# Kernel optimization log

Hardware: AMD Instinct MI355X
Metric: run time of the kernel (lower is better)

The kernel has to match this reference:

```python
import jax, jax.numpy as jnp
import numpy as np

N = 100000
E = 3200000
IN_DIM = 256
HID = 128
HID2 = 64
K = 16


def setup_inputs() -> dict:
    key = jax.random.key(0)
    ks = jax.random.split(key, 12)
    x = jax.random.normal(ks[0], (N, IN_DIM), dtype=jnp.float32)
    edge_index = jax.random.randint(ks[1], (2, E), 0, N, dtype=jnp.int64)
    edge_weight = jax.random.uniform(ks[2], (E,), dtype=jnp.float32)
    s = lambda f: 1.0 / np.sqrt(f)
    W0 = jax.random.normal(ks[3], (IN_DIM, HID), dtype=jnp.float32) * s(IN_DIM)
    b0 = jnp.zeros((HID,), jnp.float32)
    P0w = jax.random.normal(ks[4], (IN_DIM, HID), dtype=jnp.float32) * s(IN_DIM)
    P0b = jnp.zeros((HID,), jnp.float32)
    W1 = jax.random.normal(ks[5], (HID, HID2), dtype=jnp.float32) * s(HID)
    b1 = jnp.zeros((HID2,), jnp.float32)
    P1w = jax.random.normal(ks[6], (HID, HID2), dtype=jnp.float32) * s(HID)
    P1b = jnp.zeros((HID2,), jnp.float32)
    W2 = jax.random.normal(ks[7], (HID2, K), dtype=jnp.float32) * s(HID2)
    b2 = jnp.zeros((K,), jnp.float32)
    return {"x": x, "edge_index": edge_index, "edge_weight": edge_weight,
            "W0": W0, "b0": b0, "P0w": P0w, "P0b": P0b,
            "W1": W1, "b1": b1, "P1w": P1w, "P1b": P1b,
            "W2": W2, "b2": b2}


def _gcn_norm(edge_index, edge_weight, n):
    # add self loops (weight 1), symmetric normalization per PyG gcn_norm
    loop = jnp.arange(n, dtype=edge_index.dtype)
    row = jnp.concatenate([edge_index[0], loop])
    col = jnp.concatenate([edge_index[1], loop])
    w = jnp.concatenate([edge_weight, jnp.ones((n,), edge_weight.dtype)])
    deg = jax.ops.segment_sum(w, col, num_segments=n)
    dinv = jnp.where(deg > 0, jax.lax.rsqrt(deg), 0.0)
    return row, col, dinv[row] * w * dinv[col]


def reference(x, edge_index, edge_weight, W0, b0, P0w, P0b, W1, b1, P1w, P1b, W2, b2):
    n = x.shape[0]
    row, col, nw = _gcn_norm(edge_index, edge_weight, n)

    def gcn(h, W, b):
        hW = h @ W  # transform first (PyG GCNConv), then scatter-aggregate
        agg = jax.ops.segment_sum(nw[:, None] * hW[row], col, num_segments=n)
        return agg + b

    # layer 0: skip is Linear(input_dim, hidden); dropout = identity (eval)
    h = jax.nn.selu(gcn(x, W0, b0) + (x @ P0w + P0b))
    # layer 1: skip is Linear(hidden, hidden//2)
    h = jax.nn.selu(gcn(h, W1, b1) + (h @ P1w + P1b))
    # layer 2: no skip, no dropout
    h = jax.nn.selu(gcn(h, W2, b2))
    return jax.nn.softmax(h, axis=-1)
```

## Files before the change

### kernel.cpp

```cpp
#include <hip/hip_runtime.h>
#include <hip/hip_fp16.h>
#include <cmath>

#define IN_DIM 256
#define HID 128
#define HID2 64
#define SB 256
#define NODES_PB 128
#define NB_MAX 1024
#define BCAP 4608

struct __align__(8) EdgeP { int s; float w; };
union H4 { __half h[4]; uint2 u; };
union H2 { __half2 h2; uint u; };

using f16x8 = __attribute__((ext_vector_type(8))) _Float16;
using f32x4 = __attribute__((ext_vector_type(4))) float;

__device__ __forceinline__ float selu_f(float x) {
    const float scale = 1.0507009873554805f;
    const float alpha = 1.6732632423543772f;
    return x > 0.f ? scale * x : scale * alpha * expm1f(x);
}


__global__ void zero_ints(int* p, int n) {
    int i = blockIdx.x * blockDim.x + threadIdx.x;
    if (i < n) p[i] = 0;
}

__global__ void transpose_w(const float* __restrict__ B1, const float* __restrict__ B2,
                            __half* __restrict__ WT, int K, int C1, int C2) {
    int c = blockIdx.x;
    for (int k = threadIdx.x; k < K; k += blockDim.x) {
        float v = (c < C1) ? B1[(size_t)k * C1 + c] : B2[(size_t)k * C2 + (c - C1)];
        WT[(size_t)c * K + k] = __float2half(v);
    }
}

__global__ void deg_dinv(const EdgeP* __restrict__ ell, int* cnt, float* dinv, int n, int cap) {
    int wid = (blockIdx.x * blockDim.x + threadIdx.x) >> 6;
    int lane = threadIdx.x & 63;
    if (wid >= n) return;
    size_t base = (size_t)wid * cap;
    int len = min(cnt[wid], cap);
    float s = 0.f;
    for (int i = lane; i < len; i += 64) s += ell[base + i].w;
#pragma unroll
    for (int o = 32; o; o >>= 1) s += __shfl_xor(s, o);
    if (lane == 0) {
        dinv[wid] = rsqrtf(s + 1.0f);
        cnt[wid] = len;
    }
}

__global__ __launch_bounds__(256) void bin_gemm0(
    const float* __restrict__ A, const __half* __restrict__ WT,
    const float* __restrict__ bias1, const float* __restrict__ bias2,
    __half* __restrict__ outA, float* __restrict__ outB, int M,
    const int* __restrict__ ei, const float* __restrict__ ew,
    int* cnt_or_bcur, EdgeP* __restrict__ dst_buf,
    int E, int cap, int epb, int sblocks, int nb, int mode) {
    const int tid = threadIdx.x;
    __shared__ __align__(16) __half sA16[128 * 40];
    __shared__ __align__(16) __half sB16[128 * 40];

    if ((int)blockIdx.x < sblocks) {
        int lo = blockIdx.x * epb;
        int hi = min(E, lo + epb);
        if (mode == 1) {
            int* hist = (int*)sA16;
            int* gbase = (int*)sB16;
            for (int i = tid; i < nb; i += 256) hist[i] = 0;
            __syncthreads();
            for (int e = lo + tid; e < hi; e += 256)
                atomicAdd(&hist[ei[E + e] >> 7], 1);
            __syncthreads();
            for (int b = tid; b < nb; b += 256) {
                int h = hist[b];
                gbase[b] = h ? atomicAdd(&cnt_or_bcur[b], h) : 0;
                hist[b] = 0;
            }
            __syncthreads();
            for (int e = lo + tid; e < hi; e += 256) {
                int d = ei[E + e];
                int s = ei[e];
                float w = ew[e];
                int b = d >> 7;
                int lp = atomicAdd(&hist[b], 1);
                int off = gbase[b] + lp;
                if (off < BCAP) {
                    EdgeP p; p.s = (s << 7) | (d & 127); p.w = w;
                    dst_buf[(size_t)b * BCAP + off] = p;
                }
            }
        } else {
            for (int base = lo; base < hi; base += 2048) {
                int r[8], c[8], pos[8];
                float wv[8];
#pragma unroll
                for (int j = 0; j < 8; ++j) {
                    int e = base + j * 256 + tid;
                    c[j] = -1;
                    if (e < hi) { r[j] = ei[e]; c[j] = ei[E + e]; wv[j] = ew[e]; }
                }
#pragma unroll
                for (int j = 0; j < 8; ++j)
                    if (c[j] >= 0) pos[j] = atomicAdd(&cnt_or_bcur[c[j]], 1);
#pragma unroll
                for (int j = 0; j < 8; ++j)
                    if (c[j] >= 0 && pos[j] < cap) {
                        EdgeP p; p.s = r[j]; p.w = wv[j];
                        dst_buf[(size_t)c[j] * cap + pos[j]] = p;
                    }
            }
        }
        return;
    }

    const int bid = blockIdx.x - sblocks;
    const int m0 = (bid >> 1) * 128;
    const int n0 = (bid & 1) * 128;
    const int lane = tid & 63;
    const int wv = tid >> 6;
    const int wr = (wv >> 1) * 64;
    const int wc = (wv & 1) * 64;
    const int lr = lane & 15, lk = lane >> 4;

    f32x4 zero = {0.f, 0.f, 0.f, 0.f};
    f32x4 acc[4][4];
#pragma unroll
    for (int i = 0; i < 4; ++i)
#pragma unroll
        for (int j = 0; j < 4; ++j) acc[i][j] = zero;

    for (int k0 = 0; k0 < IN_DIM; k0 += 32) {
#pragma unroll
        for (int p = 0; p < 4; ++p) {
            int f4 = p * 256 + tid;
            int r = f4 >> 3;
            int kk = (f4 & 7) << 2;
            int row = m0 + r;
            float4 v = make_float4(0.f, 0.f, 0.f, 0.f);
            if (row < M) v = *(const float4*)(A + (size_t)row * IN_DIM + k0 + kk);
            H4 h;
            h.h[0] = __float2half(v.x); h.h[1] = __float2half(v.y);
            h.h[2] = __float2half(v.z); h.h[3] = __float2half(v.w);
            *(uint2*)&sA16[r * 40 + kk] = h.u;
        }
#pragma unroll
        for (int p = 0; p < 2; ++p) {
            int f = p * 256 + tid;
            int c = f >> 2;
            int kc = (f & 3) << 3;
            *(uint4*)&sB16[c * 40 + kc] =
                *(const uint4*)(WT + (size_t)(n0 + c) * IN_DIM + k0 + kc);
        }
        __syncthreads();
        f16x8 af[4], bf[4];
#pragma unroll
        for (int i = 0; i < 4; ++i)
            af[i] = *(const f16x8*)&sA16[(wr + i * 16 + lr) * 40 + lk * 8];
#pragma unroll
        for (int j = 0; j < 4; ++j)
            bf[j] = *(const f16x8*)&sB16[(wc + j * 16 + lr) * 40 + lk * 8];
#pragma unroll
        for (int i = 0; i < 4; ++i)
#pragma unroll
            for (int j = 0; j < 4; ++j)
                acc[i][j] = __builtin_amdgcn_mfma_f32_16x16x32_f16(af[i], bf[j], acc[i][j], 0, 0, 0);
        __syncthreads();
    }

    float bs[4];
    if (n0 != 0) {
#pragma unroll
        for (int j = 0; j < 4; ++j) {
            int c = wc + j * 16 + lr;
            bs[j] = bias1[c] + bias2[c];
        }
    }
#pragma unroll
    for (int i = 0; i < 4; ++i) {
        int rowb = m0 + wr + i * 16 + lk * 4;
#pragma unroll
        for (int j = 0; j < 4; ++j) {
            int col = wc + j * 16 + lr;
#pragma unroll
            for (int r = 0; r < 4; ++r) {
                int row = rowb + r;
                if (row < M) {
                    if (n0 == 0)
                        outA[(size_t)row * HID + col] = __float2half(acc[i][j][r]);
                    else
                        outB[(size_t)row * HID + col] = acc[i][j][r] + bs[j];
                }
            }
        }
    }
}

__global__ __launch_bounds__(256) void bucket_build(
    const EdgeP* __restrict__ recs, const int* __restrict__ bcur,
    EdgeP* __restrict__ ell, int* __restrict__ cnt, float* __restrict__ dinv,
    int n, int cap) {
    __shared__ int lcnt[NODES_PB];
    __shared__ float ldeg[NODES_PB];
    int b = blockIdx.x, tid = threadIdx.x;
    if (tid < NODES_PB) { lcnt[tid] = 0; ldeg[tid] = 0.f; }
    __syncthreads();
    int m = min(bcur[b], BCAP);
    const EdgeP* r = recs + (size_t)b * BCAP;
    for (int i = tid; i < m; i += 256) {
        EdgeP p = r[i];
        int dl = p.s & 127;
        int s = p.s >> 7;
        int pos = atomicAdd(&lcnt[dl], 1);
        atomicAdd(&ldeg[dl], p.w);
        if (pos < cap) {
            EdgeP q; q.s = s; q.w = p.w;
            ell[((size_t)(b * NODES_PB + dl)) * cap + pos] = q;
        }
    }
    __syncthreads();
    if (tid < NODES_PB) {
        int v = b * NODES_PB + tid;
        if (v < n) {
            cnt[v] = min(lcnt[tid], cap);
            dinv[v] = rsqrtf(ldeg[tid] + 1.0f);
        }
    }
}

__global__ __launch_bounds__(256) void gemm1_fused(
    const float* __restrict__ A, const __half* __restrict__ WT,
    const float* __restrict__ bias1, const float* __restrict__ bias2,
    __half* __restrict__ outA, float* __restrict__ outB, int M) {
    const int tid = threadIdx.x;
    __shared__ __align__(16) __half sA16[128 * 40];
    __shared__ __align__(16) __half sB16[128 * 40];
    const int m0 = blockIdx.x * 128;
    const int lane = tid & 63;
    const int wv = tid >> 6;
    const int wr = (wv >> 1) * 64;
    const int wc = (wv & 1) * 64;
    const int lr = lane & 15, lk = lane >> 4;

    f32x4 zero = {0.f, 0.f, 0.f, 0.f};
    f32x4 acc[4][4];
#pragma unroll
    for (int i = 0; i < 4; ++i)
#pragma unroll
        for (int j = 0; j < 4; ++j) acc[i][j] = zero;

    for (int k0 = 0; k0 < HID; k0 += 32) {
#pragma unroll
        for (int p = 0; p < 4; ++p) {
            int f4 = p * 256 + tid;
            int r = f4 >> 3;
            int kk = (f4 & 7) << 2;
            int row = m0 + r;
            float4 v = make_float4(0.f, 0.f, 0.f, 0.f);
            if (row < M) v = *(const float4*)(A + (size_t)row * HID + k0 + kk);
            H4 h;
            h.h[0] = __float2half(v.x); h.h[1] = __float2half(v.y);
            h.h[2] = __float2half(v.z); h.h[3] = __float2half(v.w);
            *(uint2*)&sA16[r * 40 + kk] = h.u;
        }
#pragma unroll
        for (int p = 0; p < 2; ++p) {
            int f = p * 256 + tid;
            int c = f >> 2;
            int kc = (f & 3) << 3;
            *(uint4*)&sB16[c * 40 + kc] =
                *(const uint4*)(WT + (size_t)c * HID + k0 + kc);
        }
        __syncthreads();
        f16x8 af[4], bf[4];
#pragma unroll
        for (int i = 0; i < 4; ++i)
            af[i] = *(const f16x8*)&sA16[(wr + i * 16 + lr) * 40 + lk * 8];
#pragma unroll
        for (int j = 0; j < 4; ++j)
            bf[j] = *(const f16x8*)&sB16[(wc + j * 16 + lr) * 40 + lk * 8];
#pragma unroll
        for (int i = 0; i < 4; ++i)
#pragma unroll
            for (int j = 0; j < 4; ++j)
                acc[i][j] = __builtin_amdgcn_mfma_f32_16x16x32_f16(af[i], bf[j], acc[i][j], 0, 0, 0);
        __syncthreads();
    }

    float bs[4];
    if (wc != 0) {
#pragma unroll
        for (int j = 0; j < 4; ++j) {
            int c = wc + j * 16 + lr - HID2;
            bs[j] = bias1[c] + bias2[c];
        }
    }
#pragma unroll
    for (int i = 0; i < 4; ++i) {
        int rowb = m0 + wr + i * 16 + lk * 4;
#pragma unroll
        for (int j = 0; j < 4; ++j) {
            int col = wc + j * 16 + lr;
#pragma unroll
            for (int r = 0; r < 4; ++r) {
                int row = rowb + r;
                if (row < M) {
                    if (wc == 0)
                        outA[(size_t)row * HID2 + col] = __float2half(acc[i][j][r]);
                    else
                        outB[(size_t)row * HID2 + (col - HID2)] = acc[i][j][r] + bs[j];
                }
            }
        }
    }
}

__global__ __launch_bounds__(256) void aggregate128(
    const __half* __restrict__ hW, float* __restrict__ S,
    const float* __restrict__ dinv, const int* __restrict__ cnt,
    const EdgeP* __restrict__ ell, int cap, int n) {
    int v = (blockIdx.x * 256 + threadIdx.x) >> 6;
    int lane = threadIdx.x & 63;
    if (v >= n) return;
    float di = dinv[v];
    float2 sv = *(const float2*)&S[(size_t)v * HID + lane * 2];
    H2 selfh; selfh.u = *(const uint*)&hW[(size_t)v * HID + lane * 2];
    float2 selff = __half22float2(selfh.h2);
    float selfx = sv.x + di * di * selff.x;
    float selfy = sv.y + di * di * selff.y;

    size_t base = (size_t)v * cap;
    int len = cnt[v];
    float ax[4] = {0.f, 0.f, 0.f, 0.f};
    float ay[4] = {0.f, 0.f, 0.f, 0.f};
    int i = 0;
    for (; i + 8 <= len; i += 8) {
        EdgeP p[8];
        float dv[8];
        uint h[8];
#pragma unroll
        for (int j = 0; j < 8; ++j) p[j] = ell[base + i + j];
#pragma unroll
        for (int j = 0; j < 8; ++j) {
            dv[j] = dinv[p[j].s];
            h[j] = *(const uint*)&hW[(size_t)p[j].s * HID + lane * 2];
        }
#pragma unroll
        for (int j = 0; j < 8; ++j) {
            float t = dv[j] * p[j].w;
            H2 hh; hh.u = h[j];
            float2 hf = __half22float2(hh.h2);
            ax[j & 3] = fmaf(t, hf.x, ax[j & 3]);
            ay[j & 3] = fmaf(t, hf.y, ay[j & 3]);
        }
    }
    for (; i < len; ++i) {
        EdgeP p = ell[base + i];
        float t = dinv[p.s] * p.w;
        H2 hh; hh.u = *(const uint*)&hW[(size_t)p.s * HID + lane * 2];
        float2 hf = __half22float2(hh.h2);
        ax[0] = fmaf(t, hf.x, ax[0]);
        ay[0] = fmaf(t, hf.y, ay[0]);
    }
    float sx = selfx + di * ((ax[0] + ax[1]) + (ax[2] + ax[3]));
    float sy = selfy + di * ((ay[0] + ay[1]) + (ay[2] + ay[3]));
    *(float2*)&S[(size_t)v * HID + lane * 2] = make_float2(selu_f(sx), selu_f(sy));
}

__global__ __launch_bounds__(256) void agg64_gemm2(
    const __half* __restrict__ hW, const float* __restrict__ S,
    const float* __restrict__ dinv, const int* __restrict__ cnt,
    const EdgeP* __restrict__ ell, int cap,
    const float* __restrict__ W2, __half* __restrict__ out16, int n) {
    __shared__ float sW[64 * 16];
    __shared__ float sh[4][64];
    int tid = threadIdx.x;
#pragma unroll
    for (int i = 0; i < 4; ++i) sW[i * 256 + tid] = W2[i * 256 + tid];

    int g = tid >> 6, f = tid & 63;
    int v = blockIdx.x * 4 + g;
    if (v < n) {
        float di = dinv[v];
        float self = S[(size_t)v * 64 + f] + di * di * __half2float(hW[(size_t)v * 64 + f]);
        size_t base = (size_t)v * cap;
        int len = cnt[v];
        float a[4] = {0.f, 0.f, 0.f, 0.f};
        int i = 0;
        for (; i + 8 <= len; i += 8) {
            EdgeP p[8];
            float dv[8];
            __half hv[8];
#pragma unroll
            for (int j = 0; j < 8; ++j) p[j] = ell[base + i + j];
#pragma unroll
            for (int j = 0; j < 8; ++j) {
                dv[j] = dinv[p[j].s];
                hv[j] = hW[(size_t)p[j].s * 64 + f];
            }
#pragma unroll
            for (int j = 0; j < 8; ++j)
                a[j & 3] = fmaf(dv[j] * p[j].w, __half2float(hv[j]), a[j & 3]);
        }
        for (; i < len; ++i) {
            EdgeP p = ell[base + i];
            a[0] = fmaf(dinv[p.s] * p.w, __half2float(hW[(size_t)p.s * 64 + f]), a[0]);
        }
        sh[g][f] = selu_f(self + di * ((a[0] + a[1]) + (a[2] + a[3])));
    }
    __syncthreads();
    if (v < n && f < 16) {
        float acc = 0.f;
#pragma unroll
        for (int k = 0; k < 64; ++k) acc = fmaf(sh[g][k], sW[k * 16 + f], acc);
        out16[(size_t)v * 16 + f] = __float2half(acc);
    }
}

__global__ __launch_bounds__(256) void agg_softmax(
    const __half* __restrict__ hW, const float* __restrict__ b2,
    const float* __restrict__ dinv, const int* __restrict__ cnt,
    const EdgeP* __restrict__ ell, int cap,
    float* __restrict__ out, int n) {
    int tid = threadIdx.x;
    int g = tid >> 4, f = tid & 15;
    int v = blockIdx.x * 16 + g;
    if (v >= n) return;
    float di = dinv[v];
    float acc = b2[f] + di * di * __half2float(hW[(size_t)v * 16 + f]);
    size_t base = (size_t)v * cap;
    int len = cnt[v];
    float a[4] = {0.f, 0.f, 0.f, 0.f};
    int i = 0;
    for (; i + 4 <= len; i += 4) {
        EdgeP p[4];
        float dv[4];
        __half hv[4];
#pragma unroll
        for (int j = 0; j < 4; ++j) p[j] = ell[base + i + j];
#pragma unroll
        for (int j = 0; j < 4; ++j) {
            dv[j] = dinv[p[j].s];
            hv[j] = hW[(size_t)p[j].s * 16 + f];
        }
#pragma unroll
        for (int j = 0; j < 4; ++j)
            a[j] = fmaf(dv[j] * p[j].w, __half2float(hv[j]), a[j]);
    }
    for (; i < len; ++i) {
        EdgeP p = ell[base + i];
        a[0] = fmaf(dinv[p.s] * p.w, __half2float(hW[(size_t)p.s * 16 + f]), a[0]);
    }
    acc += di * ((a[0] + a[1]) + (a[2] + a[3]));
    acc = selu_f(acc);
    float m = acc;
    m = fmaxf(m, __shfl_xor(m, 1));
    m = fmaxf(m, __shfl_xor(m, 2));
    m = fmaxf(m, __shfl_xor(m, 4));
    m = fmaxf(m, __shfl_xor(m, 8));
    float ex = expf(acc - m);
    float sm = ex;
    sm += __shfl_xor(sm, 1);
    sm += __shfl_xor(sm, 2);
    sm += __shfl_xor(sm, 4);
    sm += __shfl_xor(sm, 8);
    out[(size_t)v * 16 + f] = ex / sm;
}

extern "C" void kernel_launch(void* const* d_in, const int* in_sizes, int n_in,
                              void* d_out, int out_size, void* d_ws, size_t ws_size,
                              hipStream_t stream) {
    const float* x = (const float*)d_in[0];
    const int* ei = (const int*)d_in[1];
    const float* ew = (const float*)d_in[2];
    const float* W0 = (const float*)d_in[3];
    const float* b0 = (const float*)d_in[4];
    const float* P0w = (const float*)d_in[5];
    const float* P0b = (const float*)d_in[6];
    const float* W1 = (const float*)d_in[7];
    const float* b1 = (const float*)d_in[8];
    const float* P1w = (const float*)d_in[9];
    const float* P1b = (const float*)d_in[10];
    const float* W2 = (const float*)d_in[11];
    const float* b2 = (const float*)d_in[12];
    float* out = (float*)d_out;
    const int n = in_sizes[0] / IN_DIM;
    const int E = in_sizes[2];
    const int NB = (n + NODES_PB - 1) / NODES_PB;

    auto al = [](size_t b) { return (b + 255) & ~(size_t)255; };
    size_t oCnt = 0;
    size_t oDinv = oCnt + al((size_t)n * 4);
    size_t oBcur = oDinv + al((size_t)n * 4);
    size_t oWT0 = oBcur + al((size_t)NB_MAX * 4);
    size_t oWT1 = oWT0 + al((size_t)IN_DIM * (HID * 2) * 2);
    size_t oA = oWT1 + al((size_t)HID * HID * 2);
    size_t oB = oA + al((size_t)n * HID * 2);
    size_t oEll = oB + al((size_t)n * HID * 4);
    size_t szEll96 = al((size_t)n * 96 * 8);
    size_t szEll80 = al((size_t)n * 80 * 8);
    size_t szRec = al((size_t)NB * BCAP * 8);
    size_t szCD = al((size_t)n * HID2 * 4) + al((size_t)n * 16 * 2);
    size_t szR = szRec > szCD ? szRec : szCD;

    int cap;
    int mode;
    if (NB <= NB_MAX && oEll + szEll96 + szR <= ws_size) { cap = 96; mode = 1; }
    else if (oEll + szEll96 + szCD <= ws_size) { cap = 96; mode = 0; }
    else { cap = 80; mode = 0; }

    char* base = (char*)d_ws;
    int* cnt = (int*)(base + oCnt);
    float* dinv = (float*)(base + oDinv);
    int* bcur = (int*)(base + oBcur);
    __half* WT0 = (__half*)(base + oWT0);
    __half* WT1 = (__half*)(base + oWT1);
    __half* bufA = (__half*)(base + oA);
    float* bufB = (float*)(base + oB);
    EdgeP* ell = (EdgeP*)(base + oEll);
    size_t oR = oEll + (cap == 96 ? szEll96 : szEll80);
    EdgeP* recs = (EdgeP*)(base + oR);
    float* bufC = (float*)(base + oR);
    __half* bufD = (__half*)(base + oR + al((size_t)n * HID2 * 4));

    int gx = (n + 127) / 128;
    int gemmBlocks = gx * 2;
    int epb = (E + SB - 1) / SB;

    transpose_w<<<2 * HID, 128, 0, stream>>>(W0, P0w, WT0, IN_DIM, HID, HID);
    transpose_w<<<HID, 128, 0, stream>>>(W1, P1w, WT1, HID, HID2, HID2);

    if (mode == 1) {
        zero_ints<<<(NB_MAX + 255) / 256, 256, 0, stream>>>(bcur, NB_MAX);
        bin_gemm0<<<SB + gemmBlocks, 256, 0, stream>>>(
            x, WT0, b0, P0b, bufA, bufB, n, ei, ew, bcur, recs,
            E, cap, epb, SB, NB, 1);
        bucket_build<<<NB, 256, 0, stream>>>(recs, bcur, ell, cnt, dinv, n, cap);
    } else {
        zero_ints<<<(n + 255) / 256, 256, 0, stream>>>(cnt, n);
        bin_gemm0<<<SB + gemmBlocks, 256, 0, stream>>>(
            x, WT0, b0, P0b, bufA, bufB, n, ei, ew, cnt, ell,
            E, cap, epb, SB, NB, 0);
        int nbW = (n * 64 + 255) / 256;
        deg_dinv<<<nbW, 256, 0, stream>>>(ell, cnt, dinv, n, cap);
    }

    aggregate128<<<(n * 64 + 255) / 256, 256, 0, stream>>>(bufA, bufB, dinv, cnt, ell, cap, n);

    gemm1_fused<<<gx, 256, 0, stream>>>(bufB, WT1, b1, P1b, bufA, bufC, n);

    agg64_gemm2<<<(n + 3) / 4, 256, 0, stream>>>(bufA, bufC, dinv, cnt, ell, cap, W2, bufD, n);
    agg_softmax<<<(n + 15) / 16, 256, 0, stream>>>(bufD, b2, dinv, cnt, ell, cap, out, n);
}
```

Measured before the change: 512.0 us.

## Locally counting-sort edge chunks in LDS before scattering to buckets and ELL

The binning pass now processes edges in chunks of 4096, builds a per-chunk histogram, exclusive-scans it in one wave, and counting-sorts records in LDS so each bucket's records are written contiguously to global memory. Buckets double in size (256 nodes each), and bucket_build applies the same chunked local sort so ELL writes per node are grouped. The aim is to turn random scattered global writes into coalesced runs. The cost is extra LDS traffic, more barriers, and roughly 48KB of shared memory in bin_gemm0, which lowers occupancy for the GEMM blocks in the same kernel.

Result: faster. 495.7 us (-3.2%).

```diff
diff --git a/kernel.cpp b/kernel.cpp
--- a/kernel.cpp
+++ b/kernel.cpp
@@ -6,9 +6,10 @@
 #define HID 128
 #define HID2 64
 #define SB 256
-#define NODES_PB 128
-#define NB_MAX 1024
-#define BCAP 4608
+#define NODES_PB 256
+#define NBKT_MAX 448
+#define BCAP 9216
+#define CH 4096
 
 struct __align__(8) EdgeP { int s; float w; };
 union H4 { __half h[4]; uint2 u; };
@@ -54,6 +55,33 @@
     }
 }
 
+template <int PER>
+__device__ __forceinline__ void wave0_excl_scan(const int* lds_in, int* lds_out, int nb, int tid) {
+    if (tid < 64) {
+        int r[PER];
+        int sum = 0;
+#pragma unroll
+        for (int k = 0; k < PER; ++k) {
+            int idx = tid * PER + k;
+            int v = (idx < nb) ? lds_in[idx] : 0;
+            r[k] = sum;
+            sum += v;
+        }
+        int run = sum;
+#pragma unroll
+        for (int o = 1; o < 64; o <<= 1) {
+            int t = __shfl_up(run, o);
+            if (tid >= o) run += t;
+        }
+        int excl = run - sum;
+#pragma unroll
+        for (int k = 0; k < PER; ++k) {
+            int idx = tid * PER + k;
+            if (idx < nb) lds_out[idx] = excl + r[k];
+        }
+    }
+}
+
 __global__ __launch_bounds__(256) void bin_gemm0(
     const float* __restrict__ A, const __half* __restrict__ WT,
     const float* __restrict__ bias1, const float* __restrict__ bias2,
@@ -62,37 +90,53 @@
     int* cnt_or_bcur, EdgeP* __restrict__ dst_buf,
     int E, int cap, int epb, int sblocks, int nb, int mode) {
     const int tid = threadIdx.x;
-    __shared__ __align__(16) __half sA16[128 * 40];
-    __shared__ __align__(16) __half sB16[128 * 40];
+    __shared__ __align__(16) char smem[48128];
 
     if ((int)blockIdx.x < sblocks) {
         int lo = blockIdx.x * epb;
         int hi = min(E, lo + epb);
         if (mode == 1) {
-            int* hist = (int*)sA16;
-            int* gbase = (int*)sB16;
-            for (int i = tid; i < nb; i += 256) hist[i] = 0;
-            __syncthreads();
-            for (int e = lo + tid; e < hi; e += 256)
-                atomicAdd(&hist[ei[E + e] >> 7], 1);
-            __syncthreads();
-            for (int b = tid; b < nb; b += 256) {
-                int h = hist[b];
-                gbase[b] = h ? atomicAdd(&cnt_or_bcur[b], h) : 0;
-                hist[b] = 0;
-            }
-            __syncthreads();
-            for (int e = lo + tid; e < hi; e += 256) {
-                int d = ei[E + e];
-                int s = ei[e];
-                float w = ew[e];
-                int b = d >> 7;
-                int lp = atomicAdd(&hist[b], 1);
-                int off = gbase[b] + lp;
-                if (off < BCAP) {
-                    EdgeP p; p.s = (s << 7) | (d & 127); p.w = w;
-                    dst_buf[(size_t)b * BCAP + off] = p;
+            int* hist = (int*)smem;
+            int* off = hist + NBKT_MAX;
+            int* cur = off + NBKT_MAX;
+            int* gbase = cur + NBKT_MAX;
+            int* sortedS = gbase + NBKT_MAX;
+            float* sortedW = (float*)(sortedS + CH);
+            short* smap = (short*)(sortedW + CH);
+            for (int c0 = lo; c0 < hi; c0 += CH) {
+                int cn = min(CH, hi - c0);
+                for (int i = tid; i < nb; i += 256) hist[i] = 0;
+                __syncthreads();
+                for (int r = tid; r < cn; r += 256)
+                    atomicAdd(&hist[ei[E + c0 + r] >> 8], 1);
+                __syncthreads();
+                wave0_excl_scan<7>(hist, off, nb, tid);
+                __syncthreads();
+                for (int b = tid; b < nb; b += 256) {
+                    int h = hist[b];
+                    gbase[b] = h ? atomicAdd(&cnt_or_bcur[b], h) : 0;
+                    cur[b] = off[b];
                 }
+                __syncthreads();
+                for (int r = tid; r < cn; r += 256) {
+                    int e = c0 + r;
+                    int d = ei[E + e];
+                    int b = d >> 8;
+                    int slot = atomicAdd(&cur[b], 1);
+                    sortedS[slot] = (ei[e] << 8) | (d & 255);
+                    sortedW[slot] = ew[e];
+                    smap[slot] = (short)b;
+                }
+                __syncthreads();
+                for (int i = tid; i < cn; i += 256) {
+                    int b = smap[i];
+                    int addr = gbase[b] + (i - off[b]);
+                    if (addr < BCAP) {
+                        EdgeP p; p.s = sortedS[i]; p.w = sortedW[i];
+                        dst_buf[(size_t)b * BCAP + addr] = p;
+                    }
+                }
+                __syncthreads();
             }
         } else {
             for (int base = lo; base < hi; base += 2048) {
@@ -118,6 +162,8 @@
         return;
     }
 
+    __half* sA16 = (__half*)smem;
+    __half* sB16 = (__half*)(smem + 10240);
     const int bid = blockIdx.x - sblocks;
     const int m0 = (bid >> 1) * 128;
     const int n0 = (bid & 1) * 128;
@@ -206,29 +252,58 @@
     int n, int cap) {
     __shared__ int lcnt[NODES_PB];
     __shared__ float ldeg[NODES_PB];
+    __shared__ int chist[NODES_PB];
+    __shared__ int coff[NODES_PB];
+    __shared__ int ccur[NODES_PB];
+    __shared__ __align__(8) int sortedS[CH];
+    __shared__ float sortedW[CH];
+    __shared__ unsigned char cmap[CH];
     int b = blockIdx.x, tid = threadIdx.x;
-    if (tid < NODES_PB) { lcnt[tid] = 0; ldeg[tid] = 0.f; }
+    lcnt[tid] = 0;
+    ldeg[tid] = 0.f;
     __syncthreads();
     int m = min(bcur[b], BCAP);
-    const EdgeP* r = recs + (size_t)b * BCAP;
-    for (int i = tid; i < m; i += 256) {
-        EdgeP p = r[i];
-        int dl = p.s & 127;
-        int s = p.s >> 7;
-        int pos = atomicAdd(&lcnt[dl], 1);
-        atomicAdd(&ldeg[dl], p.w);
-        if (pos < cap) {
-            EdgeP q; q.s = s; q.w = p.w;
-            ell[((size_t)(b * NODES_PB + dl)) * cap + pos] = q;
-        }
-    }
-    __syncthreads();
-    if (tid < NODES_PB) {
-        int v = b * NODES_PB + tid;
-        if (v < n) {
-            cnt[v] = min(lcnt[tid], cap);
-            dinv[v] = rsqrtf(ldeg[tid] + 1.0f);
-        }
+    const EdgeP* rbase = recs + (size_t)b * BCAP;
+    for (int c0 = 0; c0 < m; c0 += CH) {
+        int cn = min(CH, m - c0);
+        chist[tid] = 0;
+        __syncthreads();
+        for (int i = tid; i < cn; i += 256) {
+            EdgeP p = rbase[c0 + i];
+            int dl = p.s & 255;
+            atomicAdd(&chist[dl], 1);
+            atomicAdd(&ldeg[dl], p.w);
+        }
+        __syncthreads();
+        wave0_excl_scan<4>(chist, coff, NODES_PB, tid);
+        __syncthreads();
+        ccur[tid] = coff[tid];
+        __syncthreads();
+        for (int i = tid; i < cn; i += 256) {
+            EdgeP p = rbase[c0 + i];
+            int dl = p.s & 255;
+            int slot = atomicAdd(&ccur[dl], 1);
+            sortedS[slot] = p.s >> 8;
+            sortedW[slot] = p.w;
+            cmap[slot] = (unsigned char)dl;
+        }
+        __syncthreads();
+        for (int i = tid; i < cn; i += 256) {
+            int dl = cmap[i];
+            int rank = lcnt[dl] + (i - coff[dl]);
+            if (rank < cap) {
+                EdgeP q; q.s = sortedS[i]; q.w = sortedW[i];
+                ell[((size_t)(b * NODES_PB + dl)) * cap + rank] = q;
+            }
+        }
+        __syncthreads();
+        lcnt[tid] += chist[tid];
+        __syncthreads();
+    }
+    int v = b * NODES_PB + tid;
+    if (v < n) {
+        cnt[v] = min(lcnt[tid], cap);
+        dinv[v] = rsqrtf(ldeg[tid] + 1.0f);
     }
 }
 
@@ -496,7 +571,7 @@
     size_t oCnt = 0;
     size_t oDinv = oCnt + al((size_t)n * 4);
     size_t oBcur = oDinv + al((size_t)n * 4);
-    size_t oWT0 = oBcur + al((size_t)NB_MAX * 4);
+    size_t oWT0 = oBcur + al((size_t)NBKT_MAX * 4);
     size_t oWT1 = oWT0 + al((size_t)IN_DIM * (HID * 2) * 2);
     size_t oA = oWT1 + al((size_t)HID * HID * 2);
     size_t oB = oA + al((size_t)n * HID * 2);
@@ -509,7 +584,7 @@
 
     int cap;
     int mode;
-    if (NB <= NB_MAX && oEll + szEll96 + szR <= ws_size) { cap = 96; mode = 1; }
+    if (NB <= NBKT_MAX && oEll + szEll96 + szR <= ws_size) { cap = 96; mode = 1; }
     else if (oEll + szEll96 + szCD <= ws_size) { cap = 96; mode = 0; }
     else { cap = 80; mode = 0; }
 
@@ -535,11 +610,11 @@
     transpose_w<<<HID, 128, 0, stream>>>(W1, P1w, WT1, HID, HID2, HID2);
 
     if (mode == 1) {
-        zero_ints<<<(NB_MAX + 255) / 256, 256, 0, stream>>>(bcur, NB_MAX);
+        zero_ints<<<(NBKT_MAX + 255) / 256, 256, 0, stream>>>(bcur, NBKT_MAX);
         bin_gemm0<<<SB + gemmBlocks, 256, 0, stream>>>(
             x, WT0, b0, P0b, bufA, bufB, n, ei, ew, bcur, recs,
             E, cap, epb, SB, NB, 1);
-        bucket_build<<<NB, 256, 0, stream>>>(recs, bcur, ell, cnt, dinv, n, cap);
+        bucket_build<<<NB, NODES_PB, 0, stream>>>(recs, bcur, ell, cnt, dinv, n, cap);
     } else {
         zero_ints<<<(n + 255) / 256, 256, 0, stream>>>(cnt, n);
         bin_gemm0<<<SB + gemmBlocks, 256, 0, stream>>>(
```
